# Optimization experiments

Hardware: AMD Instinct MI355X
Metric: run time of the kernel (lower is better)

The kernel has to match this reference:

```python
import jax, jax.numpy as jnp
import numpy as np

# e2m1 (nvfp4) representable magnitudes and rounding midpoints
E2M1_POS = jnp.array([0.0, 0.5, 1.0, 1.5, 2.0, 3.0, 4.0, 6.0], dtype=jnp.float32)
E2M1_BOUNDS = jnp.array([0.25, 0.75, 1.25, 1.75, 2.5, 3.5, 5.0], dtype=jnp.float32)
E2M1_TABLE = jnp.concatenate([E2M1_POS, -E2M1_POS])  # 4-bit code -> value (sign bit = bit 3)
BLOCK = 16  # nvfp4 block-scale group size


def _fp8_round(v):
    # simulate storage of block scales in float8 e4m3
    return v.astype(jnp.float8_e4m3fn).astype(jnp.float32)


def _e2m1_round(v):
    # round-to-nearest onto the e2m1 grid (|v| must be pre-clipped to <= 6)
    idx = jnp.searchsorted(E2M1_BOUNDS, jnp.abs(v))
    return jnp.sign(v) * E2M1_POS[idx]


def setup_inputs() -> dict:
    key = jax.random.key(0)
    k1, k2, k3, k4, k5 = jax.random.split(key, 5)
    M, H = 4096, 4096
    x = jax.random.normal(k1, (M, 2 * H), dtype=jnp.float32)
    w = jax.random.randint(k2, (H, H // 2), 0, 256, dtype=jnp.int32)  # packed fp4, 2 nibbles/byte
    wscale = jax.random.normal(k3, (H, H // BLOCK), dtype=jnp.float32)  # cast to fp8 inside
    wscale2 = jax.random.uniform(k4, (1,), dtype=jnp.float32)
    scale = jax.random.uniform(k5, (1,), dtype=jnp.float32)
    return {"x": x, "w": w, "wscale": wscale, "wscale2": wscale2, "scale": scale}


def reference(x, w, wscale, wscale2, scale):
    M = x.shape[0]
    H = x.shape[1] // 2
    # SiLU-and-mul
    y = jax.nn.silu(x[:, :H]) * x[:, H:]                 # [M, H]
    gs = 1.0 / scale[0]                                  # global input scale (1/self.scale)
    # NVFP4 dynamic quant: per-16-element block amax -> fp8 block scale, values -> e2m1
    yb = y.reshape(M, H // BLOCK, BLOCK)
    amax = jnp.max(jnp.abs(yb), axis=-1)                 # [M, H/16]
    sf = _fp8_round(amax * (gs / 6.0))                   # fp8-stored block scales
    inv = jnp.where(sf > 0, gs / sf, 0.0)
    q = _e2m1_round(jnp.clip(yb * inv[..., None], -6.0, 6.0))
    a_deq = (q * sf[..., None]).reshape(M, H)            # fp4 value * fp8 block scale
    # Weight side: unpack fp4 nibbles (low nibble = even k), dequant with fp8 block scales
    wu = w.astype(jnp.uint8)
    lo = (wu & 0xF).astype(jnp.int32)
    hi = (wu >> 4).astype(jnp.int32)
    codes = jnp.stack([lo, hi], axis=-1).reshape(H, H)   # [N, K]
    b_q = E2M1_TABLE[codes]
    ws = _fp8_round(wscale)                              # model stores wscale in fp8
    b_deq = b_q * jnp.repeat(ws, BLOCK, axis=1)          # [N, K]
    # cutlass_scaled_fp4_mm with alpha = scale * wscale2 undoing global scales
    alpha = scale[0] * wscale2[0]
    out = alpha * (a_deq @ b_deq.T)                      # [M, N]
    return out
```

## Files before the change

### kernel.cpp

```cpp
#include <hip/hip_runtime.h>
#include <math.h>

typedef unsigned int uint;
typedef unsigned short ushort;
typedef __attribute__((ext_vector_type(8))) short bf16x8;
typedef __attribute__((ext_vector_type(4))) float f32x4;

static constexpr int Mdim = 4096;
static constexpr int Ndim = 4096;
static constexpr int Kdim = 4096;
static constexpr int Hdim = 4096;


__device__ __forceinline__ float fp8_round(float v) {
  float a = fabsf(v);
  float q;
  if (a >= 0x1p-6f) {
    uint u = __float_as_uint(a);
    int e = (int)(u >> 23) - 127;
    float quant = __uint_as_float((uint)(e - 3 + 127) << 23);
    q = rintf(a / quant) * quant;
    q = fminf(q, 448.f);
  } else {
    q = rintf(a * 512.f) * 0x1p-9f;
  }
  return copysignf(q, v);
}

__device__ __forceinline__ float e2m1_round(float t) {
  float a = fabsf(t);
  float q;
  if (a <= 0.25f) q = 0.f;
  else if (a <= 0.75f) q = 0.5f;
  else if (a <= 1.25f) q = 1.f;
  else if (a <= 1.75f) q = 1.5f;
  else if (a <= 2.5f)  q = 2.f;
  else if (a <= 3.5f)  q = 3.f;
  else if (a <= 5.f)   q = 4.f;
  else                 q = 6.f;
  return copysignf(q, t);
}

__device__ __forceinline__ float e2m1_decode(uint c) {
  uint m = c & 7u;
  float v;
  if (m == 0u) v = 0.f;
  else if (m == 1u) v = 0.5f;
  else v = __uint_as_float(((126u + (m >> 1)) << 23) | ((m & 1u) << 22));
  return (c & 8u) ? -v : v;
}


__global__ void silu_quant_kernel(const float* __restrict__ x, ushort* __restrict__ a_deq,
                                  const float* __restrict__ scalep) {
  const int g = blockIdx.x * 256 + threadIdx.x;
  const int row = g >> 8;
  const int blk = g & 255;
  const float gs = 1.0f / scalep[0];
  const float c6 = gs / 6.0f;
  const float* gp = x + (size_t)row * (2 * Hdim) + blk * 16;
  const float* up = gp + Hdim;
  float y[16];
  float amax = 0.f;
#pragma unroll
  for (int i = 0; i < 4; ++i) {
    float4 gv = ((const float4*)gp)[i];
    float4 uv = ((const float4*)up)[i];
    float ga[4] = {gv.x, gv.y, gv.z, gv.w};
    float ua[4] = {uv.x, uv.y, uv.z, uv.w};
#pragma unroll
    for (int j = 0; j < 4; ++j) {
      float xv = ga[j];
      float sig = 1.0f / (1.0f + expf(-xv));
      float yy = xv * sig * ua[j];
      y[i * 4 + j] = yy;
      amax = fmaxf(amax, fabsf(yy));
    }
  }
  const float sf = fp8_round(amax * c6);
  uint outp[8];
  if (sf > 0.f) {
    const float inv = gs / sf;
#pragma unroll
    for (int i = 0; i < 8; ++i) {
      float t0 = fminf(fmaxf(y[2 * i] * inv, -6.f), 6.f);
      float t1 = fminf(fmaxf(y[2 * i + 1] * inv, -6.f), 6.f);
      float d0 = e2m1_round(t0) * sf;
      float d1 = e2m1_round(t1) * sf;
      outp[i] = (__float_as_uint(d0) >> 16) | ((__float_as_uint(d1) >> 16) << 16);
    }
  } else {
#pragma unroll
    for (int i = 0; i < 8; ++i) outp[i] = 0u;
  }
  uint4* dst = (uint4*)(a_deq + (size_t)row * Hdim + blk * 16);
  dst[0] = (uint4){outp[0], outp[1], outp[2], outp[3]};
  dst[1] = (uint4){outp[4], outp[5], outp[6], outp[7]};
}


__global__ void wdeq_kernel(const int* __restrict__ w, const float* __restrict__ wscale,
                            ushort* __restrict__ b_deq) {
  const int g = blockIdx.x * 256 + threadIdx.x;
  const int n = g >> 8;
  const int blk = g & 255;
  const int4* wp = (const int4*)(w + (size_t)n * (Hdim / 2) + blk * 8);
  int4 w0 = wp[0], w1 = wp[1];
  int wb[8] = {w0.x, w0.y, w0.z, w0.w, w1.x, w1.y, w1.z, w1.w};
  const float ws = fp8_round(wscale[(size_t)n * (Hdim / 16) + blk]);
  uint outp[8];
#pragma unroll
  for (int i = 0; i < 8; ++i) {
    uint byte = (uint)wb[i] & 0xFFu;
    float vlo = e2m1_decode(byte & 15u) * ws;
    float vhi = e2m1_decode(byte >> 4) * ws;
    outp[i] = (__float_as_uint(vlo) >> 16) | ((__float_as_uint(vhi) >> 16) << 16);
  }
  uint4* dst = (uint4*)(b_deq + (size_t)n * Hdim + blk * 16);
  dst[0] = (uint4){outp[0], outp[1], outp[2], outp[3]};
  dst[1] = (uint4){outp[4], outp[5], outp[6], outp[7]};
}


#define BM 256
#define BN 256
#define BK 64
#define NT (Kdim / BK)
#define TILE_E (256 * 64)

__device__ __forceinline__ void gload_lds16(const ushort* g, ushort* l) {
  __builtin_amdgcn_global_load_lds((const __attribute__((address_space(1))) void*)g,
                                   (__attribute__((address_space(3))) void*)l,
                                   16, 0, 0);
}

#define STAGE(dst, mat, goff, h, kcol)                                              \
  do {                                                                              \
    gload_lds16((mat) + (size_t)goff[(h)*2 + 0] + (kcol), (dst) + loff[(h)*2 + 0]); \
    gload_lds16((mat) + (size_t)goff[(h)*2 + 1] + (kcol), (dst) + loff[(h)*2 + 1]); \
  } while (0)

#define BAR()                                   \
  do {                                          \
    asm volatile("" ::: "memory");              \
    __builtin_amdgcn_s_barrier();               \
    asm volatile("" ::: "memory");              \
  } while (0)

__global__ __launch_bounds__(512, 2) void gemm256(const ushort* __restrict__ A,
                                                  const ushort* __restrict__ B,
                                                  float* __restrict__ C,
                                                  const float* __restrict__ scalep,
                                                  const float* __restrict__ wscale2p) {
  extern __shared__ __align__(16) ushort lds[];
  const int tid = threadIdx.x;
  const int wave = tid >> 6;
  const int lane = tid & 63;
  const int wm = wave >> 2;
  const int wn = wave & 3;
  const int fr = lane & 15;
  const int fq = lane >> 4;

  const int wg = blockIdx.x;
  const int swz = (wg & 7) * 32 + (wg >> 3);
  const int m0 = (swz >> 4) * BM;
  const int n0 = (swz & 15) * BN;

  f32x4 acc[8][4];
#pragma unroll
  for (int i = 0; i < 8; ++i)
#pragma unroll
    for (int j = 0; j < 4; ++j) acc[i][j] = (f32x4){0.f, 0.f, 0.f, 0.f};

  ushort* A0s = lds;
  ushort* A1s = lds + TILE_E;
  ushort* B0s = lds + 2 * TILE_E;
  ushort* B1s = lds + 3 * TILE_E;

  int goffA[4], goffB[4], loff[4];
#pragma unroll
  for (int h = 0; h < 2; ++h)
#pragma unroll
    for (int rr = 0; rr < 2; ++rr) {
      const int idx = h * 2 + rr;
      const int rowb = h * 128 + rr * 64 + wave * 8;
      const int trow = rowb + (lane >> 3);
      const int sc = (lane & 7) ^ (trow & 7);
      goffA[idx] = (m0 + trow) * Kdim + sc * 8;
      goffB[idx] = (n0 + trow) * Kdim + sc * 8;
      loff[idx] = rowb * 64;
    }

  const int laneAOff = (wm * 128 + fr) * 64;
  const int laneBOff = (wn * 64 + fr) * 64;
  const int xo0 = (fq ^ (fr & 7)) * 8;
  const int xo1 = ((4 + fq) ^ (fr & 7)) * 8;

  STAGE(A0s, A, goffA, 0, 0);  STAGE(A0s, A, goffA, 1, 0);
  STAGE(B0s, B, goffB, 0, 0);  STAGE(B0s, B, goffB, 1, 0);
  STAGE(B1s, B, goffB, 0, BK); STAGE(B1s, B, goffB, 1, BK);
  asm volatile("s_waitcnt vmcnt(4)" ::: "memory");
  BAR();

  bf16x8 afA[2][2], afB[2][2], bfr[4][2];
  {
    const ushort* a0 = A0s + laneAOff + xo0;
    const ushort* a1 = A0s + laneAOff + xo1;
#pragma unroll
    for (int m2 = 0; m2 < 2; ++m2) {
      afB[m2][0] = *(const bf16x8*)(a0 + m2 * 1024);
      afB[m2][1] = *(const bf16x8*)(a1 + m2 * 1024);
    }
  }

#define MFMA_Q(base, af)                                                         \
  do {                                                                           \
    __builtin_amdgcn_s_setprio(1);                                               \
    _Pragma("unroll")                                                            \
    for (int m2 = 0; m2 < 2; ++m2)                                               \
      _Pragma("unroll")                                                          \
      for (int ni = 0; ni < 4; ++ni)                                             \
        _Pragma("unroll")                                                        \
        for (int kk = 0; kk < 2; ++kk)                                           \
          acc[(base) + m2][ni] = __builtin_amdgcn_mfma_f32_16x16x32_bf16(        \
              af[m2][kk], bfr[ni][kk], acc[(base) + m2][ni], 0, 0, 0);           \
    __builtin_amdgcn_s_setprio(0);                                               \
  } while (0)

#define LGKM0()                                          \
  do {                                                   \
    asm volatile("s_waitcnt lgkmcnt(0)" ::: "memory");   \
    __builtin_amdgcn_sched_barrier(0);                   \
  } while (0)

  for (int u = 0; u < NT; ++u) {
    ushort* sA = (u & 1) ? A1s : A0s;
    ushort* sB = (u & 1) ? B1s : B0s;
    ushort* dA = (u & 1) ? A0s : A1s;
    const int kA = (u + 1) * BK;
    const int kB = (u + 2) * BK;
    const bool gA = (u + 1) < NT;
    const bool gB = (u + 2) < NT;
    const ushort* aR0 = sA + laneAOff + xo0;
    const ushort* aR1 = sA + laneAOff + xo1;

    {
      const ushort* bR0 = sB + laneBOff + xo0;
      const ushort* bR1 = sB + laneBOff + xo1;
#pragma unroll
      for (int ni = 0; ni < 4; ++ni) {
        bfr[ni][0] = *(const bf16x8*)(bR0 + ni * 1024);
        bfr[ni][1] = *(const bf16x8*)(bR1 + ni * 1024);
      }
      if (gA) STAGE(dA, A, goffA, 0, kA);
      BAR();
      LGKM0();
      MFMA_Q(0, afB);
      BAR();
    }
    {
#pragma unroll
      for (int m2 = 0; m2 < 2; ++m2) {
        afA[m2][0] = *(const bf16x8*)(aR0 + (2 + m2) * 1024);
        afA[m2][1] = *(const bf16x8*)(aR1 + (2 + m2) * 1024);
      }
      if (gA) STAGE(dA, A, goffA, 1, kA);
      BAR();
      LGKM0();
      MFMA_Q(2, afA);
      BAR();
    }
    {
#pragma unroll
      for (int m2 = 0; m2 < 2; ++m2) {
        afB[m2][0] = *(const bf16x8*)(aR0 + (4 + m2) * 1024);
        afB[m2][1] = *(const bf16x8*)(aR1 + (4 + m2) * 1024);
      }
      if (gB) STAGE(sB, B, goffB, 0, kB);
      BAR();
      LGKM0();
      MFMA_Q(4, afB);
      if (gB) asm volatile("s_waitcnt vmcnt(2)" ::: "memory");
      else    asm volatile("s_waitcnt vmcnt(0)" ::: "memory");
      BAR();
    }
    {
#pragma unroll
      for (int m2 = 0; m2 < 2; ++m2) {
        afA[m2][0] = *(const bf16x8*)(aR0 + (6 + m2) * 1024);
        afA[m2][1] = *(const bf16x8*)(aR1 + (6 + m2) * 1024);
      }
      if (gA) {
        const ushort* aN0 = dA + laneAOff + xo0;
        const ushort* aN1 = dA + laneAOff + xo1;
#pragma unroll
        for (int m2 = 0; m2 < 2; ++m2) {
          afB[m2][0] = *(const bf16x8*)(aN0 + m2 * 1024);
          afB[m2][1] = *(const bf16x8*)(aN1 + m2 * 1024);
        }
      }
      if (gB) STAGE(sB, B, goffB, 1, kB);
      BAR();
      LGKM0();
      MFMA_Q(6, afA);
      BAR();
    }
  }

  const float alpha = scalep[0] * wscale2p[0];
#pragma unroll
  for (int mi = 0; mi < 8; ++mi)
#pragma unroll
    for (int ni = 0; ni < 4; ++ni) {
      const int col = n0 + wn * 64 + ni * 16 + fr;
      const int rbase = m0 + wm * 128 + mi * 16 + fq * 4;
#pragma unroll
      for (int r = 0; r < 4; ++r)
        __builtin_nontemporal_store(alpha * acc[mi][ni][r],
                                    &C[(size_t)(rbase + r) * Ndim + col]);
    }
}


extern "C" void kernel_launch(void* const* d_in, const int* in_sizes, int n_in,
                              void* d_out, int out_size, void* d_ws, size_t ws_size,
                              hipStream_t stream) {
  const float* x       = (const float*)d_in[0];
  const int*   w       = (const int*)d_in[1];
  const float* wscale  = (const float*)d_in[2];
  const float* wscale2 = (const float*)d_in[3];
  const float* scale   = (const float*)d_in[4];
  float* out = (float*)d_out;

  ushort* a_deq = (ushort*)d_ws;
  ushort* b_deq = a_deq + (size_t)Mdim * Kdim;

  silu_quant_kernel<<<Mdim, 256, 0, stream>>>(x, a_deq, scale);
  wdeq_kernel<<<Ndim, 256, 0, stream>>>(w, wscale, b_deq);

  (void)hipFuncSetAttribute((const void*)gemm256, hipFuncAttributeMaxDynamicSharedMemorySize, 131072);
  gemm256<<<(Mdim / BM) * (Ndim / BN), 512, 131072, stream>>>(a_deq, b_deq, out, scale, wscale2);
}
```

Measured before the change: 159.7 us.

## Unroll GEMM main loop by two with double-buffered B fragments and partial LDS waits

Restructures the bf16 GEMM main loop into a 2x-unrolled body that alternates between two B-fragment register sets. The next tile's B and A fragments are prefetched during the last quarter of the current tile. Full lgkmcnt(0) waits become partial waits (lgkmcnt(4)/(12)), and one barrier per quarter is removed so LDS reads overlap with MFMAs. This adds register pressure from the extra B fragment set, and it hardcodes the trip count (NT=64) while relying on exact waitcnt accounting.

```diff
diff --git a/kernel.cpp b/kernel.cpp
--- a/kernel.cpp
+++ b/kernel.cpp
@@ -145,6 +145,84 @@
     asm volatile("" ::: "memory");              \
     __builtin_amdgcn_s_barrier();               \
     asm volatile("" ::: "memory");              \
+  } while (0)
+
+#define LGKM(n)                                                   \
+  do {                                                            \
+    asm volatile("s_waitcnt lgkmcnt(" #n ")" ::: "memory");       \
+    __builtin_amdgcn_sched_barrier(0);                            \
+  } while (0)
+
+#define MFMA16(base, AF, BFR)                                                    \
+  do {                                                                           \
+    __builtin_amdgcn_s_setprio(1);                                               \
+    _Pragma("unroll")                                                            \
+    for (int m2 = 0; m2 < 2; ++m2)                                               \
+      _Pragma("unroll")                                                          \
+      for (int ni = 0; ni < 4; ++ni)                                             \
+        _Pragma("unroll")                                                        \
+        for (int kk = 0; kk < 2; ++kk)                                           \
+          acc[(base) + m2][ni] = __builtin_amdgcn_mfma_f32_16x16x32_bf16(        \
+              AF[m2][kk], BFR[ni][kk], acc[(base) + m2][ni], 0, 0, 0);           \
+    __builtin_amdgcn_s_setprio(0);                                               \
+  } while (0)
+
+#define RD_AF(dst, aR0_, aR1_, r0)                                  \
+  do {                                                              \
+    _Pragma("unroll")                                               \
+    for (int m2 = 0; m2 < 2; ++m2) {                                \
+      dst[m2][0] = *(const bf16x8*)((aR0_) + ((r0) + m2) * 1024);   \
+      dst[m2][1] = *(const bf16x8*)((aR1_) + ((r0) + m2) * 1024);   \
+    }                                                               \
+  } while (0)
+
+#define RD_BFR(dst, bR0_, bR1_)                                     \
+  do {                                                              \
+    _Pragma("unroll")                                               \
+    for (int ni = 0; ni < 4; ++ni) {                                \
+      dst[ni][0] = *(const bf16x8*)((bR0_) + ni * 1024);            \
+      dst[ni][1] = *(const bf16x8*)((bR1_) + ni * 1024);            \
+    }                                                               \
+  } while (0)
+
+#define TILE_BODY(SA, SB, DA, OB, BFR_C, BFR_N, kA, kB, DO_A, DO_B, VMQ2, DO_N) \
+  do {                                                                          \
+    const ushort* aR0 = (SA) + laneAOff + xo0;                                  \
+    const ushort* aR1 = (SA) + laneAOff + xo1;                                  \
+       \
+    RD_AF(afB, aR0, aR1, 2);                                                    \
+    if (DO_A) STAGE((DA), A, goffA, 0, (kA));                                   \
+    LGKM(4);                                                                    \
+    MFMA16(0, afA, BFR_C);                                                      \
+    BAR();                                                                      \
+                                  \
+    RD_AF(afA, aR0, aR1, 4);                                                    \
+    if (DO_A) STAGE((DA), A, goffA, 1, (kA));                                   \
+    LGKM(4);                                                                    \
+    MFMA16(2, afB, BFR_C);                                                      \
+    BAR();                                                                      \
+                \
+    RD_AF(afB, aR0, aR1, 6);                                                    \
+    if (DO_B) STAGE((SB), B, goffB, 0, (kB));                                   \
+    LGKM(4);                                                                    \
+    MFMA16(4, afA, BFR_C);                                                      \
+    asm volatile("s_waitcnt " VMQ2 ::: "memory");                               \
+    BAR();                                                                      \
+         \
+    if (DO_N) {                                                                 \
+      const ushort* bN0 = (OB) + laneBOff + xo0;                                \
+      const ushort* bN1 = (OB) + laneBOff + xo1;                                \
+      RD_BFR(BFR_N, bN0, bN1);                                                  \
+      const ushort* aN0 = (DA) + laneAOff + xo0;                                \
+      const ushort* aN1 = (DA) + laneAOff + xo1;                                \
+      RD_AF(afA, aN0, aN1, 0);                                                  \
+      if (DO_B) STAGE((SB), B, goffB, 1, (kB));                                 \
+      LGKM(12);                                                                 \
+    } else {                                                                    \
+      LGKM(0);                                                                  \
+    }                                                                           \
+    MFMA16(6, afB, BFR_C);                                                      \
+    BAR();                                                                      \
   } while (0)
 
 __global__ __launch_bounds__(512, 2) void gemm256(const ushort* __restrict__ A,
@@ -202,110 +280,25 @@
   asm volatile("s_waitcnt vmcnt(4)" ::: "memory");
   BAR();
 
-  bf16x8 afA[2][2], afB[2][2], bfr[4][2];
+  bf16x8 afA[2][2], afB[2][2], bfrE[4][2], bfrO[4][2];
   {
+    const ushort* bR0 = B0s + laneBOff + xo0;
+    const ushort* bR1 = B0s + laneBOff + xo1;
+    RD_BFR(bfrE, bR0, bR1);
     const ushort* a0 = A0s + laneAOff + xo0;
     const ushort* a1 = A0s + laneAOff + xo1;
-#pragma unroll
-    for (int m2 = 0; m2 < 2; ++m2) {
-      afB[m2][0] = *(const bf16x8*)(a0 + m2 * 1024);
-      afB[m2][1] = *(const bf16x8*)(a1 + m2 * 1024);
-    }
-  }
-
-#define MFMA_Q(base, af)                                                         \
-  do {                                                                           \
-    __builtin_amdgcn_s_setprio(1);                                               \
-    _Pragma("unroll")                                                            \
-    for (int m2 = 0; m2 < 2; ++m2)                                               \
-      _Pragma("unroll")                                                          \
-      for (int ni = 0; ni < 4; ++ni)                                             \
-        _Pragma("unroll")                                                        \
-        for (int kk = 0; kk < 2; ++kk)                                           \
-          acc[(base) + m2][ni] = __builtin_amdgcn_mfma_f32_16x16x32_bf16(        \
-              af[m2][kk], bfr[ni][kk], acc[(base) + m2][ni], 0, 0, 0);           \
-    __builtin_amdgcn_s_setprio(0);                                               \
-  } while (0)
-
-#define LGKM0()                                          \
-  do {                                                   \
-    asm volatile("s_waitcnt lgkmcnt(0)" ::: "memory");   \
-    __builtin_amdgcn_sched_barrier(0);                   \
-  } while (0)
-
-  for (int u = 0; u < NT; ++u) {
-    ushort* sA = (u & 1) ? A1s : A0s;
-    ushort* sB = (u & 1) ? B1s : B0s;
-    ushort* dA = (u & 1) ? A0s : A1s;
-    const int kA = (u + 1) * BK;
-    const int kB = (u + 2) * BK;
-    const bool gA = (u + 1) < NT;
-    const bool gB = (u + 2) < NT;
-    const ushort* aR0 = sA + laneAOff + xo0;
-    const ushort* aR1 = sA + laneAOff + xo1;
-
-    {
-      const ushort* bR0 = sB + laneBOff + xo0;
-      const ushort* bR1 = sB + laneBOff + xo1;
-#pragma unroll
-      for (int ni = 0; ni < 4; ++ni) {
-        bfr[ni][0] = *(const bf16x8*)(bR0 + ni * 1024);
-        bfr[ni][1] = *(const bf16x8*)(bR1 + ni * 1024);
-      }
-      if (gA) STAGE(dA, A, goffA, 0, kA);
-      BAR();
-      LGKM0();
-      MFMA_Q(0, afB);
-      BAR();
-    }
-    {
-#pragma unroll
-      for (int m2 = 0; m2 < 2; ++m2) {
-        afA[m2][0] = *(const bf16x8*)(aR0 + (2 + m2) * 1024);
-        afA[m2][1] = *(const bf16x8*)(aR1 + (2 + m2) * 1024);
-      }
-      if (gA) STAGE(dA, A, goffA, 1, kA);
-      BAR();
-      LGKM0();
-      MFMA_Q(2, afA);
-      BAR();
-    }
-    {
-#pragma unroll
-      for (int m2 = 0; m2 < 2; ++m2) {
-        afB[m2][0] = *(const bf16x8*)(aR0 + (4 + m2) * 1024);
-        afB[m2][1] = *(const bf16x8*)(aR1 + (4 + m2) * 1024);
-      }
-      if (gB) STAGE(sB, B, goffB, 0, kB);
-      BAR();
-      LGKM0();
-      MFMA_Q(4, afB);
-      if (gB) asm volatile("s_waitcnt vmcnt(2)" ::: "memory");
-      else    asm volatile("s_waitcnt vmcnt(0)" ::: "memory");
-      BAR();
-    }
-    {
-#pragma unroll
-      for (int m2 = 0; m2 < 2; ++m2) {
-        afA[m2][0] = *(const bf16x8*)(aR0 + (6 + m2) * 1024);
-        afA[m2][1] = *(const bf16x8*)(aR1 + (6 + m2) * 1024);
-      }
-      if (gA) {
-        const ushort* aN0 = dA + laneAOff + xo0;
-        const ushort* aN1 = dA + laneAOff + xo1;
-#pragma unroll
-        for (int m2 = 0; m2 < 2; ++m2) {
-          afB[m2][0] = *(const bf16x8*)(aN0 + m2 * 1024);
-          afB[m2][1] = *(const bf16x8*)(aN1 + m2 * 1024);
-        }
-      }
-      if (gB) STAGE(sB, B, goffB, 1, kB);
-      BAR();
-      LGKM0();
-      MFMA_Q(6, afA);
-      BAR();
-    }
-  }
+    RD_AF(afA, a0, a1, 0);
+  }
+
+  for (int it = 0; it < 31; ++it) {
+    const int u = 2 * it;
+    TILE_BODY(A0s, B0s, A1s, B1s, bfrE, bfrO,
+              (u + 1) * BK, (u + 2) * BK, 1, 1, "vmcnt(2)", 1);
+    TILE_BODY(A1s, B1s, A0s, B0s, bfrO, bfrE,
+              (u + 2) * BK, (u + 3) * BK, 1, 1, "vmcnt(2)", 1);
+  }
+  TILE_BODY(A0s, B0s, A1s, B1s, bfrE, bfrO, 63 * BK, 0, 1, 0, "vmcnt(0)", 1);
+  TILE_BODY(A1s, B1s, A0s, B0s, bfrO, bfrE, 0, 0, 0, 0, "vmcnt(0)", 0);
 
   const float alpha = scalep[0] * wscale2p[0];
 #pragma unroll
```

Result: slower. 230.9 us (+44.6%).
